# Kernel optimization log

Hardware: AMD Instinct MI355X
Metric: run time of the kernel (lower is better)

The kernel has to match this reference:

```python
import jax, jax.numpy as jnp
import numpy as np

EPS = 1e-7  # dummy-column epsilon from stanza utils.add_dummy(eps=True)


def setup_inputs() -> dict:
    key = jax.random.key(0)
    ks = jax.random.split(key, 9)
    n_mentions, emb = 10000, 1024
    batch, n_ants, pw_emb = 1024, 64, 64
    hidden = 1024
    in_features = 3 * emb + pw_emb  # 3136
    return {
        "all_mentions": jax.random.normal(ks[0], (n_mentions, emb), jnp.float32),
        "mentions_batch": jax.random.normal(ks[1], (batch, emb), jnp.float32),
        "pw_batch": jax.random.normal(ks[2], (batch, n_ants, pw_emb), jnp.float32),
        "top_indices_batch": jax.random.randint(ks[3], (batch, n_ants), 0, n_mentions),
        "top_rough_scores_batch": jax.random.normal(ks[4], (batch, n_ants), jnp.float32),
        "W1": jax.random.normal(ks[5], (hidden, in_features), jnp.float32) * 0.02,
        "b1": jax.random.normal(ks[6], (hidden,), jnp.float32) * 0.02,
        "Wout": jax.random.normal(ks[7], (1, hidden), jnp.float32) * 0.02,
        "bout": jax.random.normal(ks[8], (1,), jnp.float32) * 0.02,
    }


def reference(all_mentions, mentions_batch, pw_batch, top_indices_batch,
              top_rough_scores_batch, W1, b1, Wout, bout):
    n_ants = pw_batch.shape[1]
    # pair matrix: [batch, n_ants, 3*emb + pw_emb]
    a = jnp.broadcast_to(mentions_batch[:, None, :],
                         (mentions_batch.shape[0], n_ants, mentions_batch.shape[1]))
    b = all_mentions[top_indices_batch]          # gather: [batch, n_ants, emb]
    pair = jnp.concatenate((a, b, a * b, pw_batch), axis=2)
    # FFNN: Linear -> LeakyReLU (dropout is identity at eval) -> Linear(->1)
    h = jax.nn.leaky_relu(jnp.einsum('bnf,hf->bnh', pair, W1) + b1, negative_slope=0.01)
    ffnn = (jnp.einsum('bnh,oh->bno', h, Wout) + bout)[..., 0]  # [batch, n_ants]
    scores = top_rough_scores_batch + ffnn
    # add dummy column with eps at position 0 -> [batch, n_ants + 1]
    dummy = jnp.full((scores.shape[0], 1), EPS, scores.dtype)
    return jnp.concatenate((dummy, scores), axis=1)
```

## Files before the change

### kernel.cpp

```cpp
#include <hip/hip_runtime.h>
#include <hip/hip_bf16.h>
#include <cstdint>
#include <cstdio>

typedef unsigned short u16;
typedef unsigned int   u32;
typedef __attribute__((ext_vector_type(8))) short bf16x8;
typedef __attribute__((ext_vector_type(4))) float f32x4;
typedef __attribute__((ext_vector_type(4))) u16   u16x4;
typedef __attribute__((ext_vector_type(8))) u16   u16x8;

#define GLOBAL_AS __attribute__((address_space(1)))
#define LDS_AS    __attribute__((address_space(3)))

static __device__ __forceinline__ u16 f2bf(float f) {
  u32 u = __builtin_bit_cast(u32, f);
  u = (u + 0x7fffu + ((u >> 16) & 1u)) >> 16;
  return (u16)u;
}
static __device__ __forceinline__ float bf2f(u16 v) {
  return __builtin_bit_cast(float, (u32)v << 16);
}
static __device__ __forceinline__ void gload_lds16(const void* g, void* l) {
  __builtin_amdgcn_global_load_lds((GLOBAL_AS u32*)g, (LDS_AS u32*)l, 16, 0, 0);
}

__global__ void k_cvt(const float* __restrict__ src, int ld, int c0,
                      int rows_src, int cols4, int total4,
                      u16* __restrict__ dst, int ldd, int dcol) {
  int gid = blockIdx.x * 256 + threadIdx.x;
  if (gid >= total4) return;
  int r = gid / cols4;
  int c = (gid - r * cols4) * 4;
  u16x4 o = {0, 0, 0, 0};
  if (r < rows_src) {
    const float4 v = *(const float4*)&src[(size_t)r * ld + c0 + c];
    o[0] = f2bf(v.x); o[1] = f2bf(v.y); o[2] = f2bf(v.z); o[3] = f2bf(v.w);
  }
  *(u16x4*)&dst[(size_t)r * ldd + dcol + c] = o;
}

__global__ void k_init(const float* __restrict__ rough,
                       const float* __restrict__ bout,
                       float* __restrict__ out) {
  int i = blockIdx.x * 256 + threadIdx.x;
  if (i >= 1024 * 65) return;
  int bi = i / 65, c = i - bi * 65;
  out[i] = (c == 0) ? 1e-7f : rough[bi * 64 + c - 1] + bout[0];
}

__global__ void k_hist(const int* __restrict__ tidx, int* __restrict__ cnt) {
  int i = blockIdx.x * 256 + threadIdx.x;
  atomicAdd(&cnt[tidx[i]], 1);
}

__global__ void k_scan(int* __restrict__ cnt) {
  __shared__ int part[512];
  int t = threadIdx.x;
  int local[20], s = 0;
#pragma unroll
  for (int i = 0; i < 20; ++i) { local[i] = cnt[t * 20 + i]; s += local[i]; }
  part[t] = s;
  __syncthreads();
  for (int off = 1; off < 512; off <<= 1) {
    int v = (t >= off) ? part[t - off] : 0;
    __syncthreads();
    part[t] += v;
    __syncthreads();
  }
  int ex = part[t] - s;
#pragma unroll
  for (int i = 0; i < 20; ++i) { int c = local[i]; cnt[t * 20 + i] = ex; ex += c; }
}

__global__ void k_scatter(const int* __restrict__ tidx, int* __restrict__ cnt,
                          int* __restrict__ perm, int* __restrict__ miS) {
  int i = blockIdx.x * 256 + threadIdx.x;
  int mi = tidx[i];
  int pos = atomicAdd(&cnt[mi], 1);
  perm[pos] = i;
  miS[pos] = mi;
}

__global__ __launch_bounds__(256)
void gemm128(const u16* __restrict__ A, int lda,
             const u16* __restrict__ B, int ldb, int Ksteps,
             u16* __restrict__ C, int ldc, const float* __restrict__ bias) {
  __shared__ u16 As[128 * 64];
  __shared__ u16 Bs[128 * 64];
  const int t = threadIdx.x;
  const int w = t >> 6, l = t & 63;
  const int wr = w >> 1, wc = w & 1;
  const int brow = blockIdx.x * 128;
  const int bcol = blockIdx.y * 128;
  const int srow = t >> 3;
  const int scol = (t & 7) * 8;
  const int gsw  = (((t & 7) ^ ((t >> 3) & 7))) * 8;

  f32x4 acc[4][4] = {};
  for (int ks = 0; ks < Ksteps; ++ks) {
    const int kb = ks * 64;
#pragma unroll
    for (int q = 0; q < 4; ++q) {
      int r = q * 32 + srow;
      gload_lds16(A + (size_t)(brow + r) * lda + kb + gsw, &As[r * 64 + scol]);
      gload_lds16(B + (size_t)(bcol + r) * ldb + kb + gsw, &Bs[r * 64 + scol]);
    }
    __syncthreads();
#pragma unroll
    for (int kk = 0; kk < 2; ++kk) {
      bf16x8 af[4], bfr[4];
      const int pg = ((kk * 4 + (l >> 4)) ^ (l & 7)) * 8;
#pragma unroll
      for (int m = 0; m < 4; ++m)
        af[m] = *(const bf16x8*)&As[(wr * 64 + m * 16 + (l & 15)) * 64 + pg];
#pragma unroll
      for (int n = 0; n < 4; ++n)
        bfr[n] = *(const bf16x8*)&Bs[(wc * 64 + n * 16 + (l & 15)) * 64 + pg];
#pragma unroll
      for (int m = 0; m < 4; ++m)
#pragma unroll
        for (int n = 0; n < 4; ++n)
          acc[m][n] = __builtin_amdgcn_mfma_f32_16x16x32_bf16(af[m], bfr[n], acc[m][n], 0, 0, 0);
    }
    __syncthreads();
  }
#pragma unroll
  for (int m = 0; m < 4; ++m)
#pragma unroll
    for (int n = 0; n < 4; ++n)
#pragma unroll
      for (int reg = 0; reg < 4; ++reg) {
        int row = brow + wr * 64 + m * 16 + (l >> 4) * 4 + reg;
        int col = bcol + wc * 64 + n * 16 + (l & 15);
        float v = acc[m][n][reg] + (bias ? bias[col] : 0.f);
        C[(size_t)row * ldc + col] = f2bf(v);
      }
}

template<bool FUSED>
__global__ __launch_bounds__(512, 1)
void gemm256(const u16* __restrict__ A, int lda,
             const u16* __restrict__ B, int ldb, int NT,
             u16* __restrict__ C, int ldc,
             const u16* __restrict__ a16, const u16* __restrict__ allm16,
             const u16* __restrict__ pwb,
             const u16* __restrict__ Aproj, const u16* __restrict__ Bproj,
             const float* __restrict__ Wout,
             const int* __restrict__ perm, const int* __restrict__ miS,
             float* __restrict__ out) {
  extern __shared__ u16 lds[];
  u16* As = lds;
  u16* Bs = lds + 2 * 2 * 128 * 64;

  const int t = threadIdx.x;
  const int l = t & 63;
  const int w = t >> 6;
  const int wrow = w >> 2, wcol = w & 3;
  const int brow = blockIdx.x * 256;
  const int bcol = blockIdx.y * 256;

  const int sr  = t >> 3;
  const int sc  = (t & 7) * 8;
  const int gsw = ((t & 7) ^ (sr & 7)) * 8;

  int mi_[2][2], pair_[2][2];
  if constexpr (FUSED) {
#pragma unroll
    for (int h = 0; h < 2; ++h)
#pragma unroll
      for (int s = 0; s < 2; ++s) {
        int lr = sr + 64 * s;
        int g  = ((lr >> 5) << 6) + h * 32 + (lr & 31);
        pair_[h][s] = perm[brow + g];
        mi_[h][s]   = miS[brow + g];
      }
  }

  auto stageA = [&](int kt, int h) {
    if (kt >= NT) return;
#pragma unroll
    for (int s = 0; s < 2; ++s) {
      int lr = sr + 64 * s;
      int g  = ((lr >> 5) << 6) + h * 32 + (lr & 31);
      gload_lds16(A + (size_t)(brow + g) * lda + kt * 64 + gsw,
                  &As[(((kt & 1) * 2 + h) * 128 + lr) * 64 + sc]);
    }
  };
  auto stageRawA = [&](int kt, int h) {
    if (kt >= NT) return;
#pragma unroll
    for (int s = 0; s < 2; ++s) {
      int lr = sr + 64 * s;
      const u16* src = (kt == NT - 1)
          ? (pwb + (size_t)pair_[h][s] * 64 + gsw)
          : (allm16 + (size_t)mi_[h][s] * 1024 + kt * 64 + gsw);
      gload_lds16(src, &As[(((kt & 1) * 2 + h) * 128 + lr) * 64 + sc]);
    }
  };
  auto stageB = [&](int kt, int h) {
    if (kt >= NT) return;
#pragma unroll
    for (int s = 0; s < 2; ++s) {
      int lr = h * 128 + sr + 64 * s;
      gload_lds16(B + (size_t)(bcol + lr) * ldb + kt * 64 + gsw,
                  &Bs[((kt & 1) * 256 + lr) * 64 + sc]);
    }
  };
  auto issueM = [&](int kt1, int h, u16x8* am) {
    if (kt1 >= NT - 1) return;
#pragma unroll
    for (int s = 0; s < 2; ++s)
      am[s] = *(const u16x8*)&a16[(size_t)(pair_[h][s] >> 6) * 1024 + kt1 * 64 + gsw];
  };
  auto rmwFin = [&](int kt1, int h, const u16x8* am) {
    if (kt1 >= NT - 1) return;
    const int cb = kt1 & 1;
#pragma unroll
    for (int s = 0; s < 2; ++s) {
      int lr = sr + 64 * s;
      u16x8 b = *(const u16x8*)&As[((cb * 2 + h) * 128 + lr) * 64 + sc];
      u16x8 o;
#pragma unroll
      for (int j = 0; j < 8; ++j) o[j] = f2bf(bf2f(am[s][j]) * bf2f(b[j]));
      *(u16x8*)&As[((cb * 2 + h) * 128 + lr) * 64 + sc] = o;
    }
  };

  f32x4 acc[8][4] = {};

  if constexpr (FUSED) {
    u16x8 am0[2];
    issueM(0, 0, am0);
    stageB(0, 0); stageB(0, 1); stageRawA(0, 0); stageRawA(0, 1);
    stageB(1, 0); stageB(1, 1);
    asm volatile("s_waitcnt vmcnt(6)" ::: "memory");
    rmwFin(0, 0, am0);
    asm volatile("s_waitcnt lgkmcnt(0)" ::: "memory");
  } else {
    stageB(0, 0); stageB(0, 1); stageA(0, 0); stageA(0, 1);
    stageB(1, 0); stageB(1, 1);
    asm volatile("s_waitcnt vmcnt(6)" ::: "memory");
  }
  __builtin_amdgcn_s_barrier();

  for (int kt = 0; kt < NT; ++kt) {
    const int cbuf = kt & 1;
    bf16x8 bfr[4][2];
    u16x8 am1[2], am0n[2];
#pragma unroll
    for (int q = 0; q < 4; ++q) {
      if (q == 0) {
#pragma unroll
        for (int n = 0; n < 4; ++n) {
          int row = wcol * 64 + n * 16 + (l & 15);
#pragma unroll
          for (int kk = 0; kk < 2; ++kk) {
            int gran = (kk * 4 + (l >> 4)) ^ (l & 7);
            bfr[n][kk] = *(const bf16x8*)&Bs[(cbuf * 256 + row) * 64 + gran * 8];
          }
        }
      }
      bf16x8 af[2][2];
#pragma unroll
      for (int m2 = 0; m2 < 2; ++m2) {
        int m = 2 * q + m2;
        int g = wrow * 128 + m * 16 + (l & 15);
        int lra = ((g >> 6) << 5) + (g & 31);
#pragma unroll
        for (int kk = 0; kk < 2; ++kk) {
          int gran = (kk * 4 + (l >> 4)) ^ (l & 7);
          af[m2][kk] = *(const bf16x8*)&As[((cbuf * 2 + (q & 1)) * 128 + lra) * 64 + gran * 8];
        }
      }

      if constexpr (FUSED) {
        if      (q == 0) { issueM(kt, 1, am1); stageRawA(kt + 1, 0); }
        else if (q == 1) { stageRawA(kt + 1, 1); }
        else if (q == 2) { stageB(kt + 2, 0); }
        else             { issueM(kt + 1, 0, am0n); stageB(kt + 2, 1); }
      } else {
        if      (q == 0) stageA(kt + 1, 0);
        else if (q == 1) stageA(kt + 1, 1);
        else if (q == 2) stageB(kt + 2, 0);
        else             stageB(kt + 2, 1);
      }

      if (q == 0) asm volatile("s_waitcnt lgkmcnt(8)" ::: "memory");
      __builtin_amdgcn_s_barrier();
      asm volatile("s_waitcnt lgkmcnt(0)" ::: "memory");
      __builtin_amdgcn_sched_barrier(0);
      __builtin_amdgcn_s_setprio(1);
#pragma unroll
      for (int m2 = 0; m2 < 2; ++m2)
#pragma unroll
        for (int n = 0; n < 4; ++n)
#pragma unroll
          for (int kk = 0; kk < 2; ++kk)
            acc[2 * q + m2][n] = __builtin_amdgcn_mfma_f32_16x16x32_bf16(
                af[m2][kk], bfr[n][kk], acc[2 * q + m2][n], 0, 0, 0);
      __builtin_amdgcn_s_setprio(0);

      if (q == 0) {
        if (kt + 1 < NT) asm volatile("s_waitcnt vmcnt(6)" ::: "memory");
        else             asm volatile("s_waitcnt vmcnt(0)" ::: "memory");
        if constexpr (FUSED) {
          rmwFin(kt, 1, am1);
          asm volatile("s_waitcnt lgkmcnt(0)" ::: "memory");
        }
      } else if (q == 3 && kt + 1 < NT) {
        if (kt + 2 < NT) asm volatile("s_waitcnt vmcnt(6)" ::: "memory");
        else             asm volatile("s_waitcnt vmcnt(2)" ::: "memory");
        if constexpr (FUSED) {
          rmwFin(kt + 1, 0, am0n);
          asm volatile("s_waitcnt lgkmcnt(0)" ::: "memory");
        }
      }
      __builtin_amdgcn_s_barrier();
    }
  }

  if constexpr (FUSED) {
    __syncthreads();
    u16* Pb = lds;
#pragma unroll
    for (int pass = 0; pass < 16; ++pass) {
      int rr = pass * 16 + (t >> 5);
      int mi = miS[brow + rr];
      int cc = (t & 31) * 8;
      int scc = cc ^ (((rr >> 1) & 7) << 3);
      gload_lds16(&Bproj[(size_t)mi * 1024 + bcol + scc], &Pb[rr * 256 + cc]);
    }
    asm volatile("s_waitcnt vmcnt(0)" ::: "memory");
    __syncthreads();

    float wo[4];
#pragma unroll
    for (int n = 0; n < 4; ++n)
      wo[n] = Wout[bcol + wcol * 64 + n * 16 + (l & 15)];
#pragma unroll
    for (int m = 0; m < 8; ++m) {
#pragma unroll
      for (int reg = 0; reg < 4; ++reg) {
        int lrow = wrow * 128 + m * 16 + (l >> 4) * 4 + reg;
        int pr = perm[brow + lrow];
        int bi = pr >> 6;
        int key = ((lrow >> 1) & 7) << 3;
        float s = 0.f;
#pragma unroll
        for (int n = 0; n < 4; ++n) {
          int lcol = wcol * 64 + n * 16 + (l & 15);
          float v = acc[m][n][reg] + bf2f(Aproj[(size_t)bi * 1024 + bcol + lcol])
                  + bf2f(Pb[lrow * 256 + (lcol ^ key)]);
          v = v > 0.f ? v : 0.01f * v;
          s += v * wo[n];
        }
        s += __shfl_xor(s, 1);
        s += __shfl_xor(s, 2);
        s += __shfl_xor(s, 4);
        s += __shfl_xor(s, 8);
        if ((l & 15) == 0)
          atomicAdd(&out[bi * 65 + 1 + (pr & 63)], s);
      }
    }
  } else {
#pragma unroll
    for (int m = 0; m < 8; ++m)
#pragma unroll
      for (int n = 0; n < 4; ++n)
#pragma unroll
        for (int reg = 0; reg < 4; ++reg) {
          int row = brow + wrow * 128 + m * 16 + (l >> 4) * 4 + reg;
          int col = bcol + wcol * 64 + n * 16 + (l & 15);
          C[(size_t)row * ldc + col] = f2bf(acc[m][n][reg]);
        }
  }
}

extern "C" void kernel_launch(void* const* d_in, const int* in_sizes, int n_in,
                              void* d_out, int out_size, void* d_ws, size_t ws_size,
                              hipStream_t stream) {
  const float* allm  = (const float*)d_in[0];
  const float* ments = (const float*)d_in[1];
  const float* pw    = (const float*)d_in[2];
  const int*   tidx  = (const int*)d_in[3];
  const float* rough = (const float*)d_in[4];
  const float* W1    = (const float*)d_in[5];
  const float* b1    = (const float*)d_in[6];
  const float* Wout  = (const float*)d_in[7];
  const float* bout  = (const float*)d_in[8];
  float* out = (float*)d_out;

  u16* A16    = (u16*)d_ws;
  u16* allm16 = A16 + 1024 * 1024;
  u16* W1a    = allm16 + 10240 * 1024;
  u16* W1b    = W1a + 1024 * 1024;
  u16* W1cp   = W1b + 1024 * 1024;
  u16* Aproj  = W1cp + 1024 * 1088;
  u16* Bproj  = Aproj + 1024 * 1024;
  u16* pwb    = Bproj + 10240 * 1024;
  int* cnt    = (int*)(pwb + (size_t)65536 * 64);
  int* perm   = cnt + 10240;
  int* miS    = perm + 65536;

  size_t need = (size_t)2 * ((size_t)1024*1024 + 10240*1024 + 1024*1024 + 1024*1024
              + 1024*1088 + 1024*1024 + 10240*1024 + (size_t)65536*64)
              + (size_t)4 * (10240 + 65536 + 65536);
  if (ws_size < need) {
    fprintf(stderr, "kernel_launch: ws_size %zu < needed %zu\n", ws_size, need);
    return;
  }

  hipFuncSetAttribute((const void*)&gemm256<false>,
                      hipFuncAttributeMaxDynamicSharedMemorySize, 131072);
  hipFuncSetAttribute((const void*)&gemm256<true>,
                      hipFuncAttributeMaxDynamicSharedMemorySize, 131072);

  hipMemsetAsync(cnt, 0, 10240 * sizeof(int), stream);
  k_hist<<<256, 256, 0, stream>>>(tidx, cnt);
  k_scan<<<1, 512, 0, stream>>>(cnt);
  k_scatter<<<256, 256, 0, stream>>>(tidx, cnt, perm, miS);

  {
    int t4;
    t4 = 1024 * 256;
    k_cvt<<<(t4 + 255) / 256, 256, 0, stream>>>(W1, 3136, 0,    1024, 256, t4, W1a, 1024, 0);
    k_cvt<<<(t4 + 255) / 256, 256, 0, stream>>>(W1, 3136, 1024, 1024, 256, t4, W1b, 1024, 0);
    k_cvt<<<(t4 + 255) / 256, 256, 0, stream>>>(W1, 3136, 2048, 1024, 256, t4, W1cp, 1088, 0);
    t4 = 1024 * 16;
    k_cvt<<<(t4 + 255) / 256, 256, 0, stream>>>(W1, 3136, 3072, 1024, 16, t4, W1cp, 1088, 1024);
    t4 = 1024 * 256;
    k_cvt<<<(t4 + 255) / 256, 256, 0, stream>>>(ments, 1024, 0, 1024, 256, t4, A16, 1024, 0);
    t4 = 10240 * 256;
    k_cvt<<<(t4 + 255) / 256, 256, 0, stream>>>(allm, 1024, 0, 10000, 256, t4, allm16, 1024, 0);
    t4 = 65536 * 16;
    k_cvt<<<(t4 + 255) / 256, 256, 0, stream>>>(pw, 64, 0, 65536, 16, t4, pwb, 64, 0);
  }

  gemm128<<<dim3(8, 8), 256, 0, stream>>>(A16, 1024, W1a, 1024, 16, Aproj, 1024, b1);
  gemm256<false><<<dim3(40, 4), 512, 131072, stream>>>(allm16, 1024, W1b, 1024, 16,
                                                       Bproj, 1024,
                                                       nullptr, nullptr, nullptr,
                                                       nullptr, nullptr, nullptr,
                                                       nullptr, nullptr, nullptr);

  k_init<<<260, 256, 0, stream>>>(rough, bout, out);

  gemm256<true><<<dim3(256, 4), 512, 131072, stream>>>(nullptr, 0, W1cp, 1088, 17,
                                                       nullptr, 0,
                                                       A16, allm16, pwb,
                                                       Aproj, Bproj, Wout,
                                                       perm, miS, out);
}
```

Measured before the change: 390.8 us.

## Stage mention-product operand via LDS and single-buffer B in fused GEMM

Measured after the change: 391.7 us. Within noise of the previous version (+0.2%).

```diff
diff --git a/kernel.cpp b/kernel.cpp
--- a/kernel.cpp
+++ b/kernel.cpp
@@ -152,6 +152,7 @@
   extern __shared__ u16 lds[];
   u16* As = lds;
   u16* Bs = lds + 2 * 2 * 128 * 64;
+  u16* Ms = Bs + 256 * 64;
 
   const int t = threadIdx.x;
   const int l = t & 63;
@@ -177,146 +178,212 @@
       }
   }
 
-  auto stageA = [&](int kt, int h) {
-    if (kt >= NT) return;
-#pragma unroll
-    for (int s = 0; s < 2; ++s) {
-      int lr = sr + 64 * s;
-      int g  = ((lr >> 5) << 6) + h * 32 + (lr & 31);
-      gload_lds16(A + (size_t)(brow + g) * lda + kt * 64 + gsw,
-                  &As[(((kt & 1) * 2 + h) * 128 + lr) * 64 + sc]);
-    }
-  };
-  auto stageRawA = [&](int kt, int h) {
-    if (kt >= NT) return;
-#pragma unroll
-    for (int s = 0; s < 2; ++s) {
-      int lr = sr + 64 * s;
-      const u16* src = (kt == NT - 1)
-          ? (pwb + (size_t)pair_[h][s] * 64 + gsw)
-          : (allm16 + (size_t)mi_[h][s] * 1024 + kt * 64 + gsw);
-      gload_lds16(src, &As[(((kt & 1) * 2 + h) * 128 + lr) * 64 + sc]);
-    }
-  };
-  auto stageB = [&](int kt, int h) {
-    if (kt >= NT) return;
-#pragma unroll
-    for (int s = 0; s < 2; ++s) {
-      int lr = h * 128 + sr + 64 * s;
-      gload_lds16(B + (size_t)(bcol + lr) * ldb + kt * 64 + gsw,
-                  &Bs[((kt & 1) * 256 + lr) * 64 + sc]);
-    }
-  };
-  auto issueM = [&](int kt1, int h, u16x8* am) {
-    if (kt1 >= NT - 1) return;
-#pragma unroll
-    for (int s = 0; s < 2; ++s)
-      am[s] = *(const u16x8*)&a16[(size_t)(pair_[h][s] >> 6) * 1024 + kt1 * 64 + gsw];
-  };
-  auto rmwFin = [&](int kt1, int h, const u16x8* am) {
-    if (kt1 >= NT - 1) return;
-    const int cb = kt1 & 1;
-#pragma unroll
-    for (int s = 0; s < 2; ++s) {
-      int lr = sr + 64 * s;
-      u16x8 b = *(const u16x8*)&As[((cb * 2 + h) * 128 + lr) * 64 + sc];
-      u16x8 o;
-#pragma unroll
-      for (int j = 0; j < 8; ++j) o[j] = f2bf(bf2f(am[s][j]) * bf2f(b[j]));
-      *(u16x8*)&As[((cb * 2 + h) * 128 + lr) * 64 + sc] = o;
-    }
-  };
-
   f32x4 acc[8][4] = {};
 
   if constexpr (FUSED) {
-    u16x8 am0[2];
-    issueM(0, 0, am0);
-    stageB(0, 0); stageB(0, 1); stageRawA(0, 0); stageRawA(0, 1);
-    stageB(1, 0); stageB(1, 1);
-    asm volatile("s_waitcnt vmcnt(6)" ::: "memory");
-    rmwFin(0, 0, am0);
+    auto stageRawA = [&](int kt, int h) {
+      if (kt >= NT) return;
+#pragma unroll
+      for (int s = 0; s < 2; ++s) {
+        int lr = sr + 64 * s;
+        const u16* src = (kt == NT - 1)
+            ? (pwb + (size_t)pair_[h][s] * 64 + gsw)
+            : (allm16 + (size_t)mi_[h][s] * 1024 + kt * 64 + gsw);
+        gload_lds16(src, &As[(((kt & 1) * 2 + h) * 128 + lr) * 64 + sc]);
+      }
+    };
+    auto stageM = [&](int kt, int h) {
+      if (kt >= NT - 1) return;
+#pragma unroll
+      for (int s = 0; s < 2; ++s) {
+        int lr = sr + 64 * s;
+        gload_lds16(a16 + (size_t)(pair_[h][s] >> 6) * 1024 + kt * 64 + gsw,
+                    &Ms[(h * 128 + lr) * 64 + sc]);
+      }
+    };
+    auto stageBt = [&](int kt, int h) {
+      if (kt >= NT) return;
+#pragma unroll
+      for (int s = 0; s < 2; ++s) {
+        int lr = h * 128 + sr + 64 * s;
+        gload_lds16(B + (size_t)(bcol + lr) * ldb + kt * 64 + gsw,
+                    &Bs[lr * 64 + sc]);
+      }
+    };
+    auto rmwFin = [&](int kt1, int h) {
+      if (kt1 >= NT - 1) return;
+      const int cb = kt1 & 1;
+#pragma unroll
+      for (int s = 0; s < 2; ++s) {
+        int lr = sr + 64 * s;
+        u16x8 b = *(const u16x8*)&As[((cb * 2 + h) * 128 + lr) * 64 + sc];
+        u16x8 a = *(const u16x8*)&Ms[(h * 128 + lr) * 64 + sc];
+        u16x8 o;
+#pragma unroll
+        for (int j = 0; j < 8; ++j) o[j] = f2bf(bf2f(a[j]) * bf2f(b[j]));
+        *(u16x8*)&As[((cb * 2 + h) * 128 + lr) * 64 + sc] = o;
+      }
+    };
+
+    stageM(0, 0); stageRawA(0, 0);
+    stageBt(0, 0); stageBt(0, 1);
+    stageM(0, 1); stageRawA(0, 1);
+    asm volatile("s_waitcnt vmcnt(8)" ::: "memory");
+    rmwFin(0, 0);
     asm volatile("s_waitcnt lgkmcnt(0)" ::: "memory");
-  } else {
-    stageB(0, 0); stageB(0, 1); stageA(0, 0); stageA(0, 1);
-    stageB(1, 0); stageB(1, 1);
-    asm volatile("s_waitcnt vmcnt(6)" ::: "memory");
-  }
-  __builtin_amdgcn_s_barrier();
-
-  for (int kt = 0; kt < NT; ++kt) {
-    const int cbuf = kt & 1;
-    bf16x8 bfr[4][2];
-    u16x8 am1[2], am0n[2];
-#pragma unroll
-    for (int q = 0; q < 4; ++q) {
-      if (q == 0) {
-#pragma unroll
-        for (int n = 0; n < 4; ++n) {
-          int row = wcol * 64 + n * 16 + (l & 15);
+    asm volatile("s_waitcnt vmcnt(4)" ::: "memory");
+    __builtin_amdgcn_s_barrier();
+
+    for (int kt = 0; kt < NT; ++kt) {
+      const int cbuf = kt & 1;
+      bf16x8 bfr[4][2];
+#pragma unroll
+      for (int q = 0; q < 4; ++q) {
+        if (q == 0) {
+#pragma unroll
+          for (int n = 0; n < 4; ++n) {
+            int row = wcol * 64 + n * 16 + (l & 15);
+#pragma unroll
+            for (int kk = 0; kk < 2; ++kk) {
+              int gran = (kk * 4 + (l >> 4)) ^ (l & 7);
+              bfr[n][kk] = *(const bf16x8*)&Bs[row * 64 + gran * 8];
+            }
+          }
+        }
+        bf16x8 af[2][2];
+#pragma unroll
+        for (int m2 = 0; m2 < 2; ++m2) {
+          int m = 2 * q + m2;
+          int g = wrow * 128 + m * 16 + (l & 15);
+          int lra = ((g >> 6) << 5) + (g & 31);
 #pragma unroll
           for (int kk = 0; kk < 2; ++kk) {
             int gran = (kk * 4 + (l >> 4)) ^ (l & 7);
-            bfr[n][kk] = *(const bf16x8*)&Bs[(cbuf * 256 + row) * 64 + gran * 8];
+            af[m2][kk] = *(const bf16x8*)&As[((cbuf * 2 + (q & 1)) * 128 + lra) * 64 + gran * 8];
           }
         }
-      }
-      bf16x8 af[2][2];
-#pragma unroll
-      for (int m2 = 0; m2 < 2; ++m2) {
-        int m = 2 * q + m2;
-        int g = wrow * 128 + m * 16 + (l & 15);
-        int lra = ((g >> 6) << 5) + (g & 31);
-#pragma unroll
-        for (int kk = 0; kk < 2; ++kk) {
-          int gran = (kk * 4 + (l >> 4)) ^ (l & 7);
-          af[m2][kk] = *(const bf16x8*)&As[((cbuf * 2 + (q & 1)) * 128 + lra) * 64 + gran * 8];
-        }
-      }
-
-      if constexpr (FUSED) {
-        if      (q == 0) { issueM(kt, 1, am1); stageRawA(kt + 1, 0); }
-        else if (q == 1) { stageRawA(kt + 1, 1); }
-        else if (q == 2) { stageB(kt + 2, 0); }
-        else             { issueM(kt + 1, 0, am0n); stageB(kt + 2, 1); }
-      } else {
+
+        if (q == 0) {
+          stageM(kt + 1, 0); stageRawA(kt + 1, 0);
+        } else if (q == 1) {
+          stageBt(kt + 1, 0); stageBt(kt + 1, 1);
+          stageM(kt + 1, 1); stageRawA(kt + 1, 1);
+        }
+
+        if (q == 0) asm volatile("s_waitcnt lgkmcnt(8)" ::: "memory");
+        __builtin_amdgcn_s_barrier();
+        asm volatile("s_waitcnt lgkmcnt(0)" ::: "memory");
+        __builtin_amdgcn_sched_barrier(0);
+        __builtin_amdgcn_s_setprio(1);
+#pragma unroll
+        for (int m2 = 0; m2 < 2; ++m2)
+#pragma unroll
+          for (int n = 0; n < 4; ++n)
+#pragma unroll
+            for (int kk = 0; kk < 2; ++kk)
+              acc[2 * q + m2][n] = __builtin_amdgcn_mfma_f32_16x16x32_bf16(
+                  af[m2][kk], bfr[n][kk], acc[2 * q + m2][n], 0, 0, 0);
+        __builtin_amdgcn_s_setprio(0);
+
+        if (q == 0) {
+          if (kt < NT - 2)       asm volatile("s_waitcnt vmcnt(4)" ::: "memory");
+          else if (kt == NT - 2) asm volatile("s_waitcnt vmcnt(2)" ::: "memory");
+          else                   asm volatile("s_waitcnt vmcnt(0)" ::: "memory");
+          rmwFin(kt, 1);
+          asm volatile("s_waitcnt lgkmcnt(0)" ::: "memory");
+        } else if (q == 3 && kt + 1 < NT) {
+          if (kt < NT - 2) asm volatile("s_waitcnt vmcnt(4)" ::: "memory");
+          else             asm volatile("s_waitcnt vmcnt(2)" ::: "memory");
+          rmwFin(kt + 1, 0);
+          asm volatile("s_waitcnt lgkmcnt(0)" ::: "memory");
+        }
+        __builtin_amdgcn_s_barrier();
+      }
+    }
+  } else {
+    auto stageA = [&](int kt, int h) {
+      if (kt >= NT) return;
+#pragma unroll
+      for (int s = 0; s < 2; ++s) {
+        int lr = sr + 64 * s;
+        int g  = ((lr >> 5) << 6) + h * 32 + (lr & 31);
+        gload_lds16(A + (size_t)(brow + g) * lda + kt * 64 + gsw,
+                    &As[(((kt & 1) * 2 + h) * 128 + lr) * 64 + sc]);
+      }
+    };
+    auto stageB2 = [&](int kt, int h) {
+      if (kt >= NT) return;
+#pragma unroll
+      for (int s = 0; s < 2; ++s) {
+        int lr = h * 128 + sr + 64 * s;
+        gload_lds16(B + (size_t)(bcol + lr) * ldb + kt * 64 + gsw,
+                    &Bs[((kt & 1) * 256 + lr) * 64 + sc]);
+      }
+    };
+
+    stageB2(0, 0); stageB2(0, 1); stageA(0, 0); stageA(0, 1);
+    stageB2(1, 0); stageB2(1, 1);
+    asm volatile("s_waitcnt vmcnt(6)" ::: "memory");
+    __builtin_amdgcn_s_barrier();
+
+    for (int kt = 0; kt < NT; ++kt) {
+      const int cbuf = kt & 1;
+      bf16x8 bfr[4][2];
+#pragma unroll
+      for (int q = 0; q < 4; ++q) {
+        if (q == 0) {
+#pragma unroll
+          for (int n = 0; n < 4; ++n) {
+            int row = wcol * 64 + n * 16 + (l & 15);
+#pragma unroll
+            for (int kk = 0; kk < 2; ++kk) {
+              int gran = (kk * 4 + (l >> 4)) ^ (l & 7);
+              bfr[n][kk] = *(const bf16x8*)&Bs[(cbuf * 256 + row) * 64 + gran * 8];
+            }
+          }
+        }
+        bf16x8 af[2][2];
+#pragma unroll
+        for (int m2 = 0; m2 < 2; ++m2) {
+          int m = 2 * q + m2;
+          int g = wrow * 128 + m * 16 + (l & 15);
+          int lra = ((g >> 6) << 5) + (g & 31);
+#pragma unroll
+          for (int kk = 0; kk < 2; ++kk) {
+            int gran = (kk * 4 + (l >> 4)) ^ (l & 7);
+            af[m2][kk] = *(const bf16x8*)&As[((cbuf * 2 + (q & 1)) * 128 + lra) * 64 + gran * 8];
+          }
+        }
+
         if      (q == 0) stageA(kt + 1, 0);
         else if (q == 1) stageA(kt + 1, 1);
-        else if (q == 2) stageB(kt + 2, 0);
-        else             stageB(kt + 2, 1);
-      }
-
-      if (q == 0) asm volatile("s_waitcnt lgkmcnt(8)" ::: "memory");
-      __builtin_amdgcn_s_barrier();
-      asm volatile("s_waitcnt lgkmcnt(0)" ::: "memory");
-      __builtin_amdgcn_sched_barrier(0);
-      __builtin_amdgcn_s_setprio(1);
-#pragma unroll
-      for (int m2 = 0; m2 < 2; ++m2)
-#pragma unroll
-        for (int n = 0; n < 4; ++n)
-#pragma unroll
-          for (int kk = 0; kk < 2; ++kk)
-            acc[2 * q + m2][n] = __builtin_amdgcn_mfma_f32_16x16x32_bf16(
-                af[m2][kk], bfr[n][kk], acc[2 * q + m2][n], 0, 0, 0);
-      __builtin_amdgcn_s_setprio(0);
-
-      if (q == 0) {
-        if (kt + 1 < NT) asm volatile("s_waitcnt vmcnt(6)" ::: "memory");
-        else             asm volatile("s_waitcnt vmcnt(0)" ::: "memory");
-        if constexpr (FUSED) {
-          rmwFin(kt, 1, am1);
-          asm volatile("s_waitcnt lgkmcnt(0)" ::: "memory");
-        }
-      } else if (q == 3 && kt + 1 < NT) {
-        if (kt + 2 < NT) asm volatile("s_waitcnt vmcnt(6)" ::: "memory");
-        else             asm volatile("s_waitcnt vmcnt(2)" ::: "memory");
-        if constexpr (FUSED) {
-          rmwFin(kt + 1, 0, am0n);
-          asm volatile("s_waitcnt lgkmcnt(0)" ::: "memory");
-        }
-      }
-      __builtin_amdgcn_s_barrier();
+        else if (q == 2) stageB2(kt + 2, 0);
+        else             stageB2(kt + 2, 1);
+
+        if (q == 0) asm volatile("s_waitcnt lgkmcnt(8)" ::: "memory");
+        __builtin_amdgcn_s_barrier();
+        asm volatile("s_waitcnt lgkmcnt(0)" ::: "memory");
+        __builtin_amdgcn_sched_barrier(0);
+        __builtin_amdgcn_s_setprio(1);
+#pragma unroll
+        for (int m2 = 0; m2 < 2; ++m2)
+#pragma unroll
+          for (int n = 0; n < 4; ++n)
+#pragma unroll
+            for (int kk = 0; kk < 2; ++kk)
+              acc[2 * q + m2][n] = __builtin_amdgcn_mfma_f32_16x16x32_bf16(
+                  af[m2][kk], bfr[n][kk], acc[2 * q + m2][n], 0, 0, 0);
+        __builtin_amdgcn_s_setprio(0);
+
+        if (q == 0) {
+          if (kt + 1 < NT) asm volatile("s_waitcnt vmcnt(6)" ::: "memory");
+          else             asm volatile("s_waitcnt vmcnt(0)" ::: "memory");
+        } else if (q == 3 && kt + 1 < NT) {
+          if (kt + 2 < NT) asm volatile("s_waitcnt vmcnt(6)" ::: "memory");
+          else             asm volatile("s_waitcnt vmcnt(2)" ::: "memory");
+        }
+        __builtin_amdgcn_s_barrier();
+      }
     }
   }
 
```
